# Kernel tuning notes

Measured on AMD Instinct MI355X. Metric: run time of the kernel, lower is better.

Reference implementation:

```python
import jax, jax.numpy as jnp
import numpy as np

N, E, B, M = 50000, 100000, 50, 50
NPG = N // B            # atoms per graph
DIN, H1, H2, DE, AAF, G = 32, 32, 64, 16, 95, 128
K, T = 3, 6             # ARMA num_stacks, num_layers
F1, F2, F3 = 64, 32, 16
EA = 2 * (M - 1)        # amino-acid edges per graph


def setup_inputs() -> dict:
    key = jax.random.key(0)
    ks = jax.random.split(key, 24)
    s = 0.05
    def w(k, shape):
        return jax.random.normal(k, shape, jnp.float32) * s
    return {
        "x": jax.random.normal(ks[0], (N, DIN), jnp.float32),
        "edge_attr": jax.random.normal(ks[1], (E, DE), jnp.float32),
        "aa_features": jax.random.normal(ks[2], (B, M, AAF), jnp.float32),
        "edge_index": jax.random.randint(ks[3], (2, E), 0, N),
        "monomer_labels": jax.random.randint(ks[4], (B, NPG), 0, M),
        "amino_edge_index": jax.random.randint(ks[5], (2, EA), 0, M),
        "W_e1": w(ks[6], (DE, DIN * H1)), "b_e1": jnp.zeros((DIN * H1,), jnp.float32),
        "root1": w(ks[7], (DIN, H1)), "bias1": jnp.zeros((H1,), jnp.float32),
        "W_e2": w(ks[8], (DE, H1 * H2)), "b_e2": jnp.zeros((H1 * H2,), jnp.float32),
        "root2": w(ks[9], (H1, H2)), "bias2": jnp.zeros((H2,), jnp.float32),
        "Wa_atom": w(ks[10], (H2, 1)), "ba_atom": jnp.zeros((1,), jnp.float32),
        "arma_init_w": w(ks[11], (K, H2 + AAF, G)),
        "arma_w": w(ks[12], (T - 1, K, G, G)),
        "arma_root_w": w(ks[13], (T, K, H2 + AAF, G)),
        "arma_bias": jnp.zeros((T, K, G), jnp.float32),
        "Wa_aa": w(ks[14], (G, 1)), "ba_aa": jnp.zeros((1,), jnp.float32),
        "W1": w(ks[15], (G, F1)), "b1": jnp.zeros((F1,), jnp.float32),
        "W2": w(ks[16], (F1, F2)), "b2": jnp.zeros((F2,), jnp.float32),
        "W3": w(ks[17], (F2, F3)), "b3": jnp.zeros((F3,), jnp.float32),
        "W4": w(ks[18], (F3, 1)), "b4": jnp.zeros((1,), jnp.float32),
    }


def _nnconv(h, src, dst, edge_attr, Wm, bm, root, bias, fin, fout):
    # NNConv (aggr='add'): edge MLP -> per-edge weight matrix, gather-matmul-scatter
    w_e = (edge_attr @ Wm + bm).reshape(-1, fin, fout)            # [E, fin, fout]
    msg = jnp.einsum('ef,efo->eo', h[src], w_e)                   # [E, fout]
    agg = jax.ops.segment_sum(msg, dst, num_segments=h.shape[0])  # scatter-add to targets
    return agg + h @ root + bias


def _forward(x, edge_attr, aa_features, W_e1, b_e1, root1, bias1, W_e2, b_e2, root2, bias2,
             Wa_atom, ba_atom, arma_init_w, arma_w, arma_root_w, arma_bias, Wa_aa, ba_aa,
             W1, b1, W2, b2, W3, b3, W4, b4, edge_index, monomer_labels, amino_edge_index):
    src, dst = edge_index[0], edge_index[1]
    h = jax.nn.relu(_nnconv(x, src, dst, edge_attr, W_e1, b_e1, root1, bias1, DIN, H1))
    h = jax.nn.relu(_nnconv(h, src, dst, edge_attr, W_e2, b_e2, root2, bias2, H1, H2))

    # per-graph attention readout over atoms -> amino-acid embeddings (scatter by monomer label)
    xg = h.reshape(B, NPG, H2)
    attn = jax.nn.softmax(xg @ Wa_atom + ba_atom, axis=1)         # softmax over atoms in graph
    wx = xg * attn
    aa = jax.vmap(lambda wxi, lbl: jax.ops.segment_sum(wxi, lbl, num_segments=M))(wx, monomer_labels)
    h_aa = jnp.concatenate([aa, aa_features], axis=-1)            # [B, M, H2+95]

    # ARMAConv: gcn_norm without self-loops on amino-acid graph (shared across graphs)
    asrc, adst = amino_edge_index[0], amino_edge_index[1]
    deg = jax.ops.segment_sum(jnp.ones((EA,), x.dtype), adst, num_segments=M)
    dinv = jnp.where(deg > 0, 1.0 / jnp.sqrt(jnp.maximum(deg, 1.0)), 0.0)
    norm = dinv[asrc] * dinv[adst]                                # [EA]

    def arma(x0):  # x0: [M, H2+95]
        out = jnp.einsum('mf,kfo->kmo', x0, arma_init_w)          # [K, M, G]
        for t in range(T):
            if t > 0:
                out = jnp.einsum('kmo,kop->kmp', out, arma_w[t - 1])
            msg = out[:, asrc] * norm[None, :, None]              # [K, EA, G]
            prop = jax.vmap(lambda m: jax.ops.segment_sum(m, adst, num_segments=M))(msg)
            rootc = jnp.einsum('mf,kfo->kmo', x0, arma_root_w[t])
            out = jax.nn.relu(prop + rootc + arma_bias[t][:, None, :])
        return out.mean(axis=0)                                   # mean over stacks -> [M, G]

    g = jax.vmap(arma)(h_aa)                                      # [B, M, G]

    # attention readout over amino acids
    attn2 = jax.nn.softmax(g @ Wa_aa + ba_aa, axis=1)
    p = jnp.sum(g * attn2, axis=1)                                # [B, G]

    p = jax.nn.relu(p @ W1 + b1)
    p = jax.nn.relu(p @ W2 + b2)
    p = jax.nn.relu(p @ W3 + b3)
    p = p @ W4 + b4
    return p.reshape(-1)                                          # [B]


def reference(x, edge_attr, aa_features, edge_index, monomer_labels, amino_edge_index,
              W_e1, b_e1, root1, bias1, W_e2, b_e2, root2, bias2, Wa_atom, ba_atom,
              arma_init_w, arma_w, arma_root_w, arma_bias, Wa_aa, ba_aa,
              W1, b1, W2, b2, W3, b3, W4, b4):
    return _forward(x, edge_attr, aa_features, W_e1, b_e1, root1, bias1, W_e2, b_e2, root2, bias2,
                    Wa_atom, ba_atom, arma_init_w, arma_w, arma_root_w, arma_bias, Wa_aa, ba_aa,
                    W1, b1, W2, b2, W3, b3, W4, b4, edge_index, monomer_labels, amino_edge_index)
```

## Files before the change

### kernel.cpp

```cpp
#include <hip/hip_runtime.h>
#include <math.h>

#define N_ATOMS 50000
#define E_EDGES 100000
#define B_G     50
#define M_M     50
#define NPG     1000
#define DIN     32
#define H1C     32
#define H2C     64
#define DEC     16
#define AAF     95
#define G_DIM   128
#define K_ST    3
#define T_L     6
#define EA_E    98
#define XDIM    159
#define NS      21
#define MPAD    64
#define GP      132
#define KP2     168
#define KW      544
#define NSB     ((N_ATOMS + 255) / 256)

typedef __attribute__((ext_vector_type(8))) short bf16x8;
typedef __attribute__((ext_vector_type(4))) float f32x4;
typedef __attribute__((ext_vector_type(4))) unsigned int u32x4;

__device__ __forceinline__ short f2bf(float f) {
    unsigned int u = __float_as_uint(f);
    unsigned int r = (u + 0x7FFFu + ((u >> 16) & 1u)) >> 16;
    return (short)r;
}
__device__ __forceinline__ float bf2f(short b) {
    return __uint_as_float(((unsigned int)(unsigned short)b) << 16);
}
__device__ __forceinline__ unsigned int cvtpk_bf16(float lo, float hi) {
    unsigned int r;
    asm("v_cvt_pk_bf16_f32 %0, %1, %2" : "=v"(r) : "v"(lo), "v"(hi));
    return r;
}

__device__ __forceinline__ void f4fma(float4& d, float s, const float4& v) {
    d.x += s * v.x; d.y += s * v.y; d.z += s * v.z; d.w += s * v.w;
}
__device__ __forceinline__ void f4add(float4& d, const float4& v) {
    d.x += v.x; d.y += v.y; d.z += v.z; d.w += v.w;
}
__device__ __forceinline__ void f4relu(float4& d) {
    d.x = fmaxf(d.x, 0.f); d.y = fmaxf(d.y, 0.f);
    d.z = fmaxf(d.z, 0.f); d.w = fmaxf(d.w, 0.f);
}

__global__ __launch_bounds__(256) void deg_count(const int* __restrict__ eidx,
                                                 int* __restrict__ deg)
{
    int e = blockIdx.x * 256 + threadIdx.x;
    if (e >= E_EDGES) return;
    atomicAdd(&deg[eidx[E_EDGES + e]], 1);
}

__global__ __launch_bounds__(256) void scan_part(const int* __restrict__ deg,
                                                 int* __restrict__ bsum)
{
    __shared__ int tmp[256];
    int tid = threadIdx.x;
    int n = blockIdx.x * 256 + tid;
    tmp[tid] = (n < N_ATOMS) ? deg[n] : 0;
    __syncthreads();
    for (int off = 128; off > 0; off >>= 1) {
        if (tid < off) tmp[tid] += tmp[tid + off];
        __syncthreads();
    }
    if (tid == 0) bsum[blockIdx.x] = tmp[0];
}

__global__ __launch_bounds__(256) void scan_mid(const int* __restrict__ bsum,
                                                int* __restrict__ bpre)
{
    __shared__ int tmp[256];
    int tid = threadIdx.x;
    int v = (tid < NSB) ? bsum[tid] : 0;
    tmp[tid] = v;
    __syncthreads();
    for (int off = 1; off < 256; off <<= 1) {
        int t = tmp[tid];
        int add = (tid >= off) ? tmp[tid - off] : 0;
        __syncthreads();
        tmp[tid] = t + add;
        __syncthreads();
    }
    if (tid < NSB) bpre[tid] = tmp[tid] - v;
}

__global__ __launch_bounds__(256) void scan_out(int* __restrict__ deg_off,
                                                const int* __restrict__ bpre)
{
    __shared__ int tmp[256];
    int tid = threadIdx.x;
    int n = blockIdx.x * 256 + tid;
    int v = (n < N_ATOMS) ? deg_off[n] : 0;
    tmp[tid] = v;
    __syncthreads();
    for (int off = 1; off < 256; off <<= 1) {
        int t = tmp[tid];
        int add = (tid >= off) ? tmp[tid - off] : 0;
        __syncthreads();
        tmp[tid] = t + add;
        __syncthreads();
    }
    int incl = tmp[tid];
    int base = bpre[blockIdx.x];
    if (n < N_ATOMS) deg_off[n] = base + incl - v;
    if (n == N_ATOMS - 1) deg_off[N_ATOMS] = base + incl;
}

__global__ __launch_bounds__(256) void fill_order(const int* __restrict__ eidx,
                                                  const int* __restrict__ off,
                                                  int* __restrict__ cursor,
                                                  int* __restrict__ order)
{
    int e = blockIdx.x * 256 + threadIdx.x;
    if (e >= E_EDGES) return;
    int d = eidx[E_EDGES + e];
    int pos = atomicAdd(&cursor[d], 1);
    order[off[d] + pos] = e;
}

template<int FOUT>
__global__ __launch_bounds__(256) void prep_we(
    const float* __restrict__ We, const float* __restrict__ be,
    short* __restrict__ WB)
{
    int idx = blockIdx.x * 256 + threadIdx.x;
    if (idx >= FOUT * KW) return;
    int o = idx / KW, k = idx - o * KW;
    float v = (k < 512) ? We[(size_t)k * FOUT + o]
                        : be[(size_t)(k - 512) * FOUT + o];
    WB[(size_t)o * KW + k] = f2bf(v);
}

template<int FOUT, int NTT, int WGRP, int MTB>
__global__ __launch_bounds__(256) void edge_msg_v2(
    const float* __restrict__ h, const float* __restrict__ ea,
    const int* __restrict__ eidx, const short* __restrict__ WB,
    float* __restrict__ msg)
{
    constexpr int KS = 17;
    int tid  = threadIdx.x;
    int lane = tid & 63, wave = tid >> 6;
    int l16  = lane & 15, quad = lane >> 4;
    int nt   = wave % NTT, tg = wave / NTT;
    int ebase = blockIdx.x * (MTB * 16);

    bf16x8 Bfr[KS];
    {
        const short* wb = WB + (size_t)(nt * 16 + l16) * KW;
        #pragma unroll
        for (int ks = 0; ks < KS; ++ks)
            Bfr[ks] = *(const bf16x8*)(wb + ks * 32 + quad * 8);
    }

    for (int t = tg; t < MTB; t += WGRP) {
        int e  = ebase + t * 16 + l16;
        int es = (e < E_EDGES) ? e : (E_EDGES - 1);
        int s  = eidx[es];
        float4 h0 = *(const float4*)(h + (size_t)s * 32 + quad * 8);
        float4 h1 = *(const float4*)(h + (size_t)s * 32 + quad * 8 + 4);
        float hf[8] = {h0.x, h0.y, h0.z, h0.w, h1.x, h1.y, h1.z, h1.w};
        float4 e0 = *(const float4*)(ea + (size_t)es * DEC);
        float4 e1 = *(const float4*)(ea + (size_t)es * DEC + 4);
        float4 e2 = *(const float4*)(ea + (size_t)es * DEC + 8);
        float4 e3 = *(const float4*)(ea + (size_t)es * DEC + 12);
        float eaf[16] = {e0.x, e0.y, e0.z, e0.w, e1.x, e1.y, e1.z, e1.w,
                         e2.x, e2.y, e2.z, e2.w, e3.x, e3.y, e3.z, e3.w};

        f32x4 acc = (f32x4){0.f, 0.f, 0.f, 0.f};
        #pragma unroll
        for (int ks = 0; ks < KS; ++ks) {
            u32x4 av;
            if (ks < DEC) {
                float fac = eaf[ks];
                #pragma unroll
                for (int j = 0; j < 4; ++j)
                    av[j] = cvtpk_bf16(fac * hf[2 * j], fac * hf[2 * j + 1]);
            } else {
                #pragma unroll
                for (int j = 0; j < 4; ++j)
                    av[j] = cvtpk_bf16(hf[2 * j], hf[2 * j + 1]);
            }
            bf16x8 a = __builtin_bit_cast(bf16x8, av);
            acc = __builtin_amdgcn_mfma_f32_16x16x32_bf16(a, Bfr[ks], acc, 0, 0, 0);
        }
        int erb = ebase + t * 16 + quad * 4;
        float* mp = msg + (size_t)erb * FOUT + nt * 16 + l16;
        #pragma unroll
        for (int r = 0; r < 4; ++r) {
            if (erb + r < E_EDGES) mp[(size_t)r * FOUT] = acc[r];
        }
    }
}

template<int FIN, int FOUT>
__global__ __launch_bounds__(256) void gather_update(
    const float* __restrict__ msg, const int* __restrict__ off,
    const int* __restrict__ order, const float* __restrict__ hin,
    const float* __restrict__ root, const float* __restrict__ bias,
    float* __restrict__ hout)
{
    constexpr int NPB = 256 / FOUT;
    __shared__ float rlds[FIN][FOUT];
    __shared__ float hlds[NPB][FIN];
    int tid = threadIdx.x;
    for (int i = tid; i < FIN * FOUT / 4; i += 256) {
        *(float4*)&rlds[0][i * 4] = *(const float4*)(root + i * 4);
    }
    int nb = blockIdx.x * NPB;
    for (int i = tid; i < NPB * FIN; i += 256) {
        int ln = i / FIN, f = i % FIN;
        int n = nb + ln;
        hlds[ln][f] = (n < N_ATOMS) ? hin[(size_t)n * FIN + f] : 0.f;
    }
    __syncthreads();

    int ln = tid / FOUT, o = tid % FOUT;
    int n = nb + ln;
    if (n >= N_ATOMS) return;
    float acc = bias[o];
    #pragma unroll 8
    for (int f = 0; f < FIN; ++f) acc += hlds[ln][f] * rlds[f][o];
    int j0 = off[n], j1 = off[n + 1];
    for (int j = j0; j < j1; ++j) {
        int e = order[j];
        acc += msg[(size_t)e * FOUT + o];
    }
    hout[(size_t)n * FOUT + o] = fmaxf(acc, 0.f);
}

__global__ __launch_bounds__(256) void atom_score(
    const float* __restrict__ h2, const float* __restrict__ wa,
    const float* __restrict__ ba, float* __restrict__ sc)
{
    __shared__ float hl[128][65];
    int nb = blockIdx.x * 128;
    int tid = threadIdx.x;
    for (int i = tid; i < 128 * 16; i += 256) {
        int r = i >> 4, c4 = i & 15;
        int n = nb + r;
        float4 v = (n < N_ATOMS) ? *(const float4*)(h2 + (size_t)n * H2C + c4 * 4)
                                 : make_float4(0.f, 0.f, 0.f, 0.f);
        *(float4*)&hl[r][c4 * 4] = v;
    }
    __syncthreads();
    if (tid < 128) {
        int n = nb + tid;
        if (n < N_ATOMS) {
            float sv = ba[0];
            #pragma unroll 8
            for (int o = 0; o < H2C; ++o) sv += hl[tid][o] * wa[o];
            sc[n] = sv;
        }
    }
}

__global__ __launch_bounds__(256) void atom_aggregate(
    const float* __restrict__ h2, const float* __restrict__ sc,
    const int* __restrict__ labels, const float* __restrict__ aaf,
    float* __restrict__ h_aa)
{
    int bx = blockIdx.x, tid = threadIdx.x;
    if (bx < 2 * B_G) {
        __shared__ float aa8[8][M_M][32];
        __shared__ float red[256];
        int b = bx >> 1, half = bx & 1;
        int g = tid >> 5, o = tid & 31;
        const float* sb = sc + (size_t)b * NPG;
        float lmax = -1e30f;
        for (int n = tid; n < NPG; n += 256) lmax = fmaxf(lmax, sb[n]);
        red[tid] = lmax;
        __syncthreads();
        for (int off = 128; off > 0; off >>= 1) {
            if (tid < off) red[tid] = fmaxf(red[tid], red[tid + off]);
            __syncthreads();
        }
        float mx = red[0];
        __syncthreads();
        float lsum = 0.f;
        for (int n = tid; n < NPG; n += 256) lsum += expf(sb[n] - mx);
        red[tid] = lsum;
        __syncthreads();
        for (int off = 128; off > 0; off >>= 1) {
            if (tid < off) red[tid] += red[tid + off];
            __syncthreads();
        }
        float inv = 1.f / red[0];
        __syncthreads();
        for (int i = tid; i < 8 * M_M * 32; i += 256) ((float*)aa8)[i] = 0.f;
        __syncthreads();
        const float* hb = h2 + (size_t)b * NPG * H2C + half * 32;
        for (int n = g; n < NPG; n += 8) {
            int lbl = labels[b * NPG + n];
            float w = expf(sb[n] - mx) * inv;
            float hvv = hb[(size_t)n * H2C + o];
            aa8[g][lbl][o] += hvv * w;
        }
        __syncthreads();
        float* ob = h_aa + (size_t)b * M_M * XDIM + half * 32;
        for (int i = tid; i < M_M * 32; i += 256) {
            int m = i >> 5, oo = i & 31;
            float v = 0.f;
            #pragma unroll
            for (int gg = 0; gg < 8; ++gg) v += aa8[gg][m][oo];
            ob[m * XDIM + oo] = v;
        }
    } else {
        int b = bx - 2 * B_G;
        const float* ab = aaf + (size_t)b * M_M * AAF;
        float* ob = h_aa + (size_t)b * M_M * XDIM + H2C;
        for (int i = tid; i < M_M * AAF; i += 256) {
            int m = i / AAF, j = i - m * AAF;
            ob[m * XDIM + j] = ab[i];
        }
    }
}

__global__ void aa_norm_kernel(const int* __restrict__ aei,
                               int* __restrict__ aa_off,
                               int* __restrict__ aa_src,
                               float* __restrict__ aa_nrm)
{
    __shared__ int   sdeg[M_M];
    __shared__ int   scur[M_M];
    __shared__ float sdinv[M_M];
    __shared__ int   soff[M_M + 1];
    int tid = threadIdx.x;
    if (tid < M_M) { sdeg[tid] = 0; scur[tid] = 0; }
    __syncthreads();
    if (tid < EA_E) atomicAdd(&sdeg[aei[EA_E + tid]], 1);
    __syncthreads();
    if (tid < M_M) {
        float dv = (float)sdeg[tid];
        sdinv[tid] = (dv > 0.f) ? (1.f / sqrtf(fmaxf(dv, 1.f))) : 0.f;
    }
    __syncthreads();
    if (tid == 0) {
        soff[0] = 0;
        for (int m = 0; m < M_M; ++m) soff[m + 1] = soff[m] + sdeg[m];
    }
    __syncthreads();
    if (tid < EA_E) {
        int ss = aei[tid], dd = aei[EA_E + tid];
        int pos = atomicAdd(&scur[dd], 1);
        int idx = soff[dd] + pos;
        aa_src[idx] = ss;
        aa_nrm[idx] = sdinv[ss] * sdinv[dd];
    }
    if (tid < M_M + 1) aa_off[tid] = soff[tid];
}

__global__ __launch_bounds__(256) void prep_wt(
    const float* __restrict__ init_w, const float* __restrict__ root_w,
    short* __restrict__ Wtb)
{
    int idx = blockIdx.x * 256 + threadIdx.x;
    if (idx >= NS * XDIM * G_DIM) return;
    int s = idx / (XDIM * G_DIM);
    int rem = idx - s * XDIM * G_DIM;
    int k = rem / G_DIM, n = rem - k * G_DIM;
    float v = (s < K_ST) ? init_w[idx]
                         : root_w[(size_t)(s - K_ST) * XDIM * G_DIM + rem];
    Wtb[(size_t)s * G_DIM * KP2 + n * KP2 + k] = f2bf(v);
}

__global__ __launch_bounds__(256) void prep_aw(
    const float* __restrict__ arma_w, short* __restrict__ Wab)
{
    int idx = blockIdx.x * 256 + threadIdx.x;
    if (idx >= (T_L - 1) * K_ST * G_DIM * G_DIM) return;
    int slot = idx / (G_DIM * G_DIM);
    int rem = idx - slot * G_DIM * G_DIM;
    int p = rem / G_DIM, n = rem - p * G_DIM;
    Wab[(size_t)slot * G_DIM * G_DIM + n * G_DIM + p] = f2bf(arma_w[idx]);
}

__global__ __launch_bounds__(256) void prep_x0(
    const float* __restrict__ h_aa, short* __restrict__ x0b)
{
    int idx = blockIdx.x * 256 + threadIdx.x;
    if (idx >= B_G * MPAD * KP2) return;
    int b = idx / (MPAD * KP2);
    int rem = idx - b * MPAD * KP2;
    int m = rem / KP2, k = rem - m * KP2;
    float v = (m < M_M && k < XDIM) ? h_aa[((size_t)b * M_M + m) * XDIM + k] : 0.f;
    x0b[idx] = f2bf(v);
}

__global__ __launch_bounds__(256) void rc_gemm_mfma(
    const short* __restrict__ x0b, const short* __restrict__ Wtb,
    float* __restrict__ RC)
{
    int b = blockIdx.x / NS, s = blockIdx.x % NS;
    int tid = threadIdx.x;
    int lane = tid & 63, wave = tid >> 6;
    int l16 = lane & 15, quad = lane >> 4;
    const short* xa = x0b + (size_t)b * MPAD * KP2 + (wave * 16 + l16) * KP2;
    const short* wb = Wtb + (size_t)s * G_DIM * KP2;

    f32x4 acc[8];
    #pragma unroll
    for (int nt = 0; nt < 8; ++nt) acc[nt] = (f32x4){0.f, 0.f, 0.f, 0.f};

    #pragma unroll
    for (int ks = 0; ks < 5; ++ks) {
        bf16x8 a = *(const bf16x8*)(xa + ks * 32 + quad * 8);
        #pragma unroll
        for (int nt = 0; nt < 8; ++nt) {
            bf16x8 bf = *(const bf16x8*)(wb + (nt * 16 + l16) * KP2 + ks * 32 + quad * 8);
            acc[nt] = __builtin_amdgcn_mfma_f32_16x16x32_bf16(a, bf, acc[nt], 0, 0, 0);
        }
    }
    float* op = RC + (size_t)(b * NS + s) * M_M * G_DIM;
    #pragma unroll
    for (int nt = 0; nt < 8; ++nt) {
        #pragma unroll
        for (int r = 0; r < 4; ++r) {
            int m = wave * 16 + quad * 4 + r;
            if (m < M_M)
                op[m * G_DIM + nt * 16 + l16] = acc[nt][r];
        }
    }
}

__global__ __launch_bounds__(512) void arma_iter(
    const float* __restrict__ RC, const short* __restrict__ Wab,
    const float* __restrict__ arma_bias,
    const int* __restrict__ aa_off, const int* __restrict__ aa_src,
    const float* __restrict__ aa_nrm, float* __restrict__ gfull)
{
    __shared__ float Abuf[MPAD][GP];
    __shared__ float Bbuf[MPAD][GP];
    __shared__ int   s_off[M_M + 1];
    __shared__ int   s_src[EA_E];
    __shared__ float s_nrm[EA_E];
    int b = blockIdx.x / K_ST, k = blockIdx.x % K_ST;
    int tid = threadIdx.x;
    int oi = tid & 15, mi = tid >> 4;
    int c0 = oi * 4, c1 = 64 + oi * 4;
    int lane = tid & 63, wave = tid >> 6;
    int l16 = lane & 15, quad = lane >> 4;
    int mt = wave >> 1, nh = wave & 1;

    const float* rcb = RC + (size_t)b * NS * M_M * G_DIM;
    if (tid < M_M + 1) s_off[tid] = aa_off[tid];
    if (tid < EA_E) { s_src[tid] = aa_src[tid]; s_nrm[tid] = aa_nrm[tid]; }

    for (int i = tid; i < MPAD * G_DIM; i += 512) {
        int m = i >> 7, o = i & 127;
        Abuf[m][o] = (m < M_M) ? rcb[(size_t)k * M_M * G_DIM + i] : 0.f;
        Bbuf[m][o] = 0.f;
    }
    __syncthreads();

    for (int t = 0; t < T_L; ++t) {
        if (t > 0) {
            const short* aw = Wab + (size_t)((t - 1) * K_ST + k) * G_DIM * G_DIM;
            f32x4 acc[4];
            #pragma unroll
            for (int nt = 0; nt < 4; ++nt) acc[nt] = (f32x4){0.f, 0.f, 0.f, 0.f};
            #pragma unroll
            for (int ks = 0; ks < 4; ++ks) {
                bf16x8 a;
                const float* ap = &Bbuf[mt * 16 + l16][ks * 32 + quad * 8];
                #pragma unroll
                for (int j = 0; j < 8; ++j) a[j] = f2bf(ap[j]);
                #pragma unroll
                for (int nt = 0; nt < 4; ++nt) {
                    int n0 = (nh * 4 + nt) * 16 + l16;
                    bf16x8 bf = *(const bf16x8*)(aw + n0 * G_DIM + ks * 32 + quad * 8);
                    acc[nt] = __builtin_amdgcn_mfma_f32_16x16x32_bf16(a, bf, acc[nt], 0, 0, 0);
                }
            }
            #pragma unroll
            for (int nt = 0; nt < 4; ++nt) {
                #pragma unroll
                for (int r = 0; r < 4; ++r) {
                    Abuf[mt * 16 + quad * 4 + r][(nh * 4 + nt) * 16 + l16] = acc[nt][r];
                }
            }
            __syncthreads();
        }
        const float* rct = rcb + (size_t)(K_ST + t * K_ST + k) * M_M * G_DIM;
        const float* bb  = arma_bias + ((size_t)t * K_ST + k) * G_DIM;
        float4 bias0 = *(const float4*)(bb + c0);
        float4 bias1 = *(const float4*)(bb + c1);
        #pragma unroll
        for (int r = 0; r < 2; ++r) {
            int m = mi * 2 + r;
            if (m < M_M) {
                const float* rr = rct + (size_t)m * G_DIM;
                float4 v0 = bias0, v1 = bias1;
                f4add(v0, *(const float4*)(rr + c0));
                f4add(v1, *(const float4*)(rr + c1));
                int j0 = s_off[m], j1 = s_off[m + 1];
                for (int j = j0; j < j1; ++j) {
                    float nv = s_nrm[j];
                    const float* ap = &Abuf[s_src[j]][0];
                    f4fma(v0, nv, *(const float4*)(ap + c0));
                    f4fma(v1, nv, *(const float4*)(ap + c1));
                }
                f4relu(v0);
                f4relu(v1);
                *(float4*)&Bbuf[m][c0] = v0;
                *(float4*)&Bbuf[m][c1] = v1;
            }
        }
        __syncthreads();
    }
    float* gb = gfull + ((size_t)(b * K_ST + k)) * M_M * G_DIM;
    for (int i = tid; i < M_M * G_DIM; i += 512) {
        int m = i >> 7, o = i & 127;
        gb[i] = Bbuf[m][o];
    }
}

__global__ __launch_bounds__(128) void aa_readout_mlp(
    const float* __restrict__ gfull, const float* __restrict__ wa,
    const float* __restrict__ ba,
    const float* __restrict__ W1, const float* __restrict__ b1,
    const float* __restrict__ W2, const float* __restrict__ b2,
    const float* __restrict__ W3, const float* __restrict__ b3,
    const float* __restrict__ W4, const float* __restrict__ b4,
    float* __restrict__ out)
{
    __shared__ float g[M_M][G_DIM + 1];
    __shared__ float s2[M_M];
    __shared__ float p[G_DIM];
    __shared__ float r1[64], r2[32], r3[16];
    int b = blockIdx.x, tid = threadIdx.x;
    const float* g0 = gfull + (size_t)b * K_ST * M_M * G_DIM;
    for (int i = tid; i < M_M * G_DIM; i += 128) {
        int m = i >> 7, o = i & 127;
        g[m][o] = (g0[i] + g0[M_M*G_DIM + i] + g0[2*M_M*G_DIM + i]) * (1.f/3.f);
    }
    __syncthreads();
    if (tid < M_M) {
        float sv = ba[0];
        for (int o = 0; o < G_DIM; ++o) sv += g[tid][o] * wa[o];
        s2[tid] = sv;
    }
    __syncthreads();
    if (tid == 0) {
        float mx = -1e30f;
        for (int m = 0; m < M_M; ++m) mx = fmaxf(mx, s2[m]);
        float den = 0.f;
        for (int m = 0; m < M_M; ++m) den += expf(s2[m] - mx);
        float inv = 1.f / den;
        for (int m = 0; m < M_M; ++m) s2[m] = expf(s2[m] - mx) * inv;
    }
    __syncthreads();
    {
        float pv = 0.f;
        for (int m = 0; m < M_M; ++m) pv += g[m][tid] * s2[m];
        p[tid] = pv;
    }
    __syncthreads();
    if (tid < 64) {
        float v = b1[tid];
        for (int i = 0; i < 128; ++i) v += p[i] * W1[i * 64 + tid];
        r1[tid] = fmaxf(v, 0.f);
    }
    __syncthreads();
    if (tid < 32) {
        float v = b2[tid];
        for (int i = 0; i < 64; ++i) v += r1[i] * W2[i * 32 + tid];
        r2[tid] = fmaxf(v, 0.f);
    }
    __syncthreads();
    if (tid < 16) {
        float v = b3[tid];
        for (int i = 0; i < 32; ++i) v += r2[i] * W3[i * 16 + tid];
        r3[tid] = fmaxf(v, 0.f);
    }
    __syncthreads();
    if (tid == 0) {
        float v = b4[0];
        for (int i = 0; i < 16; ++i) v += r3[i] * W4[i];
        out[b] = v;
    }
}

extern "C" void kernel_launch(void* const* d_in, const int* in_sizes, int n_in,
                              void* d_out, int out_size, void* d_ws, size_t ws_size,
                              hipStream_t stream)
{
    (void)in_sizes; (void)n_in; (void)out_size; (void)ws_size;
    const float* x            = (const float*)d_in[0];
    const float* edge_attr    = (const float*)d_in[1];
    const float* aa_features  = (const float*)d_in[2];
    const int*   edge_index   = (const int*)  d_in[3];
    const int*   mono_labels  = (const int*)  d_in[4];
    const int*   amino_ei     = (const int*)  d_in[5];
    const float* W_e1 = (const float*)d_in[6];
    const float* b_e1 = (const float*)d_in[7];
    const float* root1= (const float*)d_in[8];
    const float* bias1= (const float*)d_in[9];
    const float* W_e2 = (const float*)d_in[10];
    const float* b_e2 = (const float*)d_in[11];
    const float* root2= (const float*)d_in[12];
    const float* bias2= (const float*)d_in[13];
    const float* Wa_atom = (const float*)d_in[14];
    const float* ba_atom = (const float*)d_in[15];
    const float* arma_init_w = (const float*)d_in[16];
    const float* arma_w      = (const float*)d_in[17];
    const float* arma_root_w = (const float*)d_in[18];
    const float* arma_bias   = (const float*)d_in[19];
    const float* Wa_aa = (const float*)d_in[20];
    const float* ba_aa = (const float*)d_in[21];
    const float* W1 = (const float*)d_in[22];
    const float* b1 = (const float*)d_in[23];
    const float* W2 = (const float*)d_in[24];
    const float* b2 = (const float*)d_in[25];
    const float* W3 = (const float*)d_in[26];
    const float* b3 = (const float*)d_in[27];
    const float* W4 = (const float*)d_in[28];
    const float* b4 = (const float*)d_in[29];

    float* ws = (float*)d_ws;
    float* h1    = ws;
    float* h2    = h1   + (size_t)N_ATOMS * H1C;
    float* h_aa  = h2   + (size_t)N_ATOMS * H2C;
    float* sc    = h_aa + (size_t)B_G * M_M * XDIM;
    int*   aa_off = (int*)(sc + (size_t)B_G * NPG);
    int*   aa_src = aa_off + (M_M + 1);
    float* aa_nrm = (float*)(aa_src + EA_E);
    int*   deg_off = (int*)(aa_nrm + EA_E);
    int*   cursor  = deg_off + (N_ATOMS + 1);
    int*   order   = cursor + N_ATOMS;
    int*   bsum    = order + E_EDGES;
    int*   bpre    = bsum + 256;
    float* RC    = (float*)(bpre + 256);
    float* gfull = RC + (size_t)B_G * NS * M_M * G_DIM;
    short* Wtb   = (short*)((((uintptr_t)(gfull + (size_t)B_G * K_ST * M_M * G_DIM)) + 15)
                            & ~(uintptr_t)15);
    short* x0b   = Wtb + (size_t)NS * G_DIM * KP2;
    short* Wab   = x0b + (size_t)B_G * MPAD * KP2;
    short* WB1   = Wab + (size_t)(T_L - 1) * K_ST * G_DIM * G_DIM;
    short* WB2   = WB1 + (size_t)H1C * KW;
    float* msg   = RC;

    (void)hipMemsetAsync(deg_off, 0, (2 * N_ATOMS + 1) * sizeof(int), stream);

    int eblocks = (E_EDGES + 255) / 256;

    deg_count<<<eblocks, 256, 0, stream>>>(edge_index, deg_off);
    scan_part<<<NSB, 256, 0, stream>>>(deg_off, bsum);
    scan_mid<<<1, 256, 0, stream>>>(bsum, bpre);
    scan_out<<<NSB, 256, 0, stream>>>(deg_off, bpre);
    fill_order<<<eblocks, 256, 0, stream>>>(edge_index, deg_off, cursor, order);

    prep_we<H1C><<<(H1C * KW + 255) / 256, 256, 0, stream>>>(W_e1, b_e1, WB1);
    prep_we<H2C><<<(H2C * KW + 255) / 256, 256, 0, stream>>>(W_e2, b_e2, WB2);
    prep_wt<<<(NS * XDIM * G_DIM + 255) / 256, 256, 0, stream>>>(
        arma_init_w, arma_root_w, Wtb);
    prep_aw<<<((T_L - 1) * K_ST * G_DIM * G_DIM + 255) / 256, 256, 0, stream>>>(
        arma_w, Wab);

    edge_msg_v2<H1C, 2, 2, 8><<<(E_EDGES + 127) / 128, 256, 0, stream>>>(
        x, edge_attr, edge_index, WB1, msg);
    gather_update<DIN, H1C><<<(N_ATOMS + 7) / 8, 256, 0, stream>>>(
        msg, deg_off, order, x, root1, bias1, h1);
    edge_msg_v2<H2C, 4, 1, 4><<<(E_EDGES + 63) / 64, 256, 0, stream>>>(
        h1, edge_attr, edge_index, WB2, msg);
    gather_update<H1C, H2C><<<(N_ATOMS + 3) / 4, 256, 0, stream>>>(
        msg, deg_off, order, h1, root2, bias2, h2);

    atom_score<<<(N_ATOMS + 127) / 128, 256, 0, stream>>>(h2, Wa_atom, ba_atom, sc);
    atom_aggregate<<<3 * B_G, 256, 0, stream>>>(h2, sc, mono_labels, aa_features, h_aa);

    aa_norm_kernel<<<1, 128, 0, stream>>>(amino_ei, aa_off, aa_src, aa_nrm);
    prep_x0<<<(B_G * MPAD * KP2 + 255) / 256, 256, 0, stream>>>(h_aa, x0b);
    rc_gemm_mfma<<<B_G * NS, 256, 0, stream>>>(x0b, Wtb, RC);
    arma_iter<<<B_G * K_ST, 512, 0, stream>>>(RC, Wab, arma_bias,
                                              aa_off, aa_src, aa_nrm, gfull);
    aa_readout_mlp<<<B_G, 128, 0, stream>>>(gfull, Wa_aa, ba_aa, W1, b1, W2, b2, W3, b3, W4, b4,
                                            (float*)d_out);
}
```

Baseline: 360.2 us.

## Split atom aggregation into softmax, sliced scatter, and fused x0 finalize kernels

Replaces the per-graph atom_aggregate kernel (100 blocks each looping over all 1000 atoms) with three kernels. A per-graph softmax writes normalized weights in place, and a scatter kernel splits each graph into 10 atom slices across 500 blocks that write partial per-monomer sums. A finalize kernel reduces the partials and directly produces the padded bf16 x0 buffer, absorbing prep_x0 and the aa_features copy. This raises parallelism and removes the h_aa intermediate, at the cost of an extra launch and a partial-sum buffer round trip through memory (aliased onto RC).

Measured after the change: 336.7 us. -6.5%, faster.

```diff
diff --git a/kernel.cpp b/kernel.cpp
--- a/kernel.cpp
+++ b/kernel.cpp
@@ -21,6 +21,8 @@
 #define GP      132
 #define KP2     168
 #define KW      544
+#define SLC     10
+#define APB     100
 #define NSB     ((N_ATOMS + 255) / 256)
 
 typedef __attribute__((ext_vector_type(8))) short bf16x8;
@@ -263,65 +265,83 @@
     }
 }
 
-__global__ __launch_bounds__(256) void atom_aggregate(
-    const float* __restrict__ h2, const float* __restrict__ sc,
-    const int* __restrict__ labels, const float* __restrict__ aaf,
-    float* __restrict__ h_aa)
-{
-    int bx = blockIdx.x, tid = threadIdx.x;
-    if (bx < 2 * B_G) {
-        __shared__ float aa8[8][M_M][32];
-        __shared__ float red[256];
-        int b = bx >> 1, half = bx & 1;
-        int g = tid >> 5, o = tid & 31;
-        const float* sb = sc + (size_t)b * NPG;
-        float lmax = -1e30f;
-        for (int n = tid; n < NPG; n += 256) lmax = fmaxf(lmax, sb[n]);
-        red[tid] = lmax;
-        __syncthreads();
-        for (int off = 128; off > 0; off >>= 1) {
-            if (tid < off) red[tid] = fmaxf(red[tid], red[tid + off]);
-            __syncthreads();
-        }
-        float mx = red[0];
-        __syncthreads();
-        float lsum = 0.f;
-        for (int n = tid; n < NPG; n += 256) lsum += expf(sb[n] - mx);
-        red[tid] = lsum;
-        __syncthreads();
-        for (int off = 128; off > 0; off >>= 1) {
-            if (tid < off) red[tid] += red[tid + off];
-            __syncthreads();
-        }
-        float inv = 1.f / red[0];
-        __syncthreads();
-        for (int i = tid; i < 8 * M_M * 32; i += 256) ((float*)aa8)[i] = 0.f;
-        __syncthreads();
-        const float* hb = h2 + (size_t)b * NPG * H2C + half * 32;
-        for (int n = g; n < NPG; n += 8) {
-            int lbl = labels[b * NPG + n];
-            float w = expf(sb[n] - mx) * inv;
-            float hvv = hb[(size_t)n * H2C + o];
-            aa8[g][lbl][o] += hvv * w;
-        }
-        __syncthreads();
-        float* ob = h_aa + (size_t)b * M_M * XDIM + half * 32;
-        for (int i = tid; i < M_M * 32; i += 256) {
-            int m = i >> 5, oo = i & 31;
-            float v = 0.f;
+__global__ __launch_bounds__(256) void graph_softmax(float* __restrict__ sc)
+{
+    __shared__ float red[256];
+    int b = blockIdx.x, tid = threadIdx.x;
+    float* sb = sc + (size_t)b * NPG;
+    float lmax = -1e30f;
+    for (int n = tid; n < NPG; n += 256) lmax = fmaxf(lmax, sb[n]);
+    red[tid] = lmax;
+    __syncthreads();
+    for (int off = 128; off > 0; off >>= 1) {
+        if (tid < off) red[tid] = fmaxf(red[tid], red[tid + off]);
+        __syncthreads();
+    }
+    float mx = red[0];
+    __syncthreads();
+    float lsum = 0.f;
+    for (int n = tid; n < NPG; n += 256) lsum += expf(sb[n] - mx);
+    red[tid] = lsum;
+    __syncthreads();
+    for (int off = 128; off > 0; off >>= 1) {
+        if (tid < off) red[tid] += red[tid + off];
+        __syncthreads();
+    }
+    float inv = 1.f / red[0];
+    __syncthreads();
+    for (int n = tid; n < NPG; n += 256) sb[n] = expf(sb[n] - mx) * inv;
+}
+
+__global__ __launch_bounds__(256) void atom_scatter(
+    const float* __restrict__ h2, const float* __restrict__ wn,
+    const int* __restrict__ labels, float* __restrict__ partial)
+{
+    __shared__ float aa4[4][M_M][H2C];
+    int b = blockIdx.x / SLC, s = blockIdx.x % SLC;
+    int tid = threadIdx.x;
+    int wave = tid >> 6, lane = tid & 63;
+    for (int i = tid; i < 4 * M_M * H2C; i += 256) ((float*)aa4)[i] = 0.f;
+    __syncthreads();
+    int nbase = s * APB;
+    const float* hb = h2 + (size_t)b * NPG * H2C;
+    #pragma unroll 5
+    for (int it = 0; it < APB / 4; ++it) {
+        int n = nbase + it * 4 + wave;
+        int lbl = labels[b * NPG + n];
+        float w = wn[(size_t)b * NPG + n];
+        float hv = hb[(size_t)n * H2C + lane];
+        aa4[wave][lbl][lane] += hv * w;
+    }
+    __syncthreads();
+    float* pb = partial + (size_t)(b * SLC + s) * M_M * H2C;
+    for (int i = tid; i < M_M * H2C; i += 256) {
+        float v = ((float*)aa4)[i] + ((float*)aa4)[M_M * H2C + i]
+                + ((float*)aa4)[2 * M_M * H2C + i] + ((float*)aa4)[3 * M_M * H2C + i];
+        pb[i] = v;
+    }
+}
+
+__global__ __launch_bounds__(256) void x0_finalize(
+    const float* __restrict__ partial, const float* __restrict__ aaf,
+    short* __restrict__ x0b)
+{
+    int idx = blockIdx.x * 256 + threadIdx.x;
+    if (idx >= B_G * MPAD * KP2) return;
+    int b = idx / (MPAD * KP2);
+    int rem = idx - b * (MPAD * KP2);
+    int m = rem / KP2, k = rem - m * KP2;
+    float v = 0.f;
+    if (m < M_M) {
+        if (k < H2C) {
+            const float* pb = partial + (size_t)b * SLC * M_M * H2C + m * H2C + k;
             #pragma unroll
-            for (int gg = 0; gg < 8; ++gg) v += aa8[gg][m][oo];
-            ob[m * XDIM + oo] = v;
-        }
-    } else {
-        int b = bx - 2 * B_G;
-        const float* ab = aaf + (size_t)b * M_M * AAF;
-        float* ob = h_aa + (size_t)b * M_M * XDIM + H2C;
-        for (int i = tid; i < M_M * AAF; i += 256) {
-            int m = i / AAF, j = i - m * AAF;
-            ob[m * XDIM + j] = ab[i];
-        }
-    }
+            for (int s = 0; s < SLC; ++s) v += pb[(size_t)s * (M_M * H2C)];
+        } else if (k < XDIM) {
+            v = aaf[((size_t)b * M_M + m) * AAF + (k - H2C)];
+        }
+    }
+    x0b[idx] = f2bf(v);
 }
 
 __global__ void aa_norm_kernel(const int* __restrict__ aei,
@@ -381,18 +401,6 @@
     int rem = idx - slot * G_DIM * G_DIM;
     int p = rem / G_DIM, n = rem - p * G_DIM;
     Wab[(size_t)slot * G_DIM * G_DIM + n * G_DIM + p] = f2bf(arma_w[idx]);
-}
-
-__global__ __launch_bounds__(256) void prep_x0(
-    const float* __restrict__ h_aa, short* __restrict__ x0b)
-{
-    int idx = blockIdx.x * 256 + threadIdx.x;
-    if (idx >= B_G * MPAD * KP2) return;
-    int b = idx / (MPAD * KP2);
-    int rem = idx - b * MPAD * KP2;
-    int m = rem / KP2, k = rem - m * KP2;
-    float v = (m < M_M && k < XDIM) ? h_aa[((size_t)b * M_M + m) * XDIM + k] : 0.f;
-    x0b[idx] = f2bf(v);
 }
 
 __global__ __launch_bounds__(256) void rc_gemm_mfma(
@@ -647,6 +655,8 @@
     short* WB1   = Wab + (size_t)(T_L - 1) * K_ST * G_DIM * G_DIM;
     short* WB2   = WB1 + (size_t)H1C * KW;
     float* msg   = RC;
+    float* partial = RC;
+    (void)h_aa;
 
     (void)hipMemsetAsync(deg_off, 0, (2 * N_ATOMS + 1) * sizeof(int), stream);
 
@@ -675,10 +685,12 @@
         msg, deg_off, order, h1, root2, bias2, h2);
 
     atom_score<<<(N_ATOMS + 127) / 128, 256, 0, stream>>>(h2, Wa_atom, ba_atom, sc);
-    atom_aggregate<<<3 * B_G, 256, 0, stream>>>(h2, sc, mono_labels, aa_features, h_aa);
+    graph_softmax<<<B_G, 256, 0, stream>>>(sc);
+    atom_scatter<<<B_G * SLC, 256, 0, stream>>>(h2, sc, mono_labels, partial);
+    x0_finalize<<<(B_G * MPAD * KP2 + 255) / 256, 256, 0, stream>>>(
+        partial, aa_features, x0b);
 
     aa_norm_kernel<<<1, 128, 0, stream>>>(amino_ei, aa_off, aa_src, aa_nrm);
-    prep_x0<<<(B_G * MPAD * KP2 + 255) / 256, 256, 0, stream>>>(h_aa, x0b);
     rc_gemm_mfma<<<B_G * NS, 256, 0, stream>>>(x0b, Wtb, RC);
     arma_iter<<<B_G * K_ST, 512, 0, stream>>>(RC, Wab, arma_bias,
                                               aa_off, aa_src, aa_nrm, gfull);
```
